# Optimization experiments

Hardware: AMD Instinct MI355X
Metric: run time of the kernel (lower is better)

## Reference

```python
import jax, jax.numpy as jnp
import numpy as np

N = 50000          # nodes in current snapshot
NUM = 20000        # nodes persisting from past snapshots (args.number[now-past])
PAST = 3           # history length
D = 128            # first_dim == hidden_dim == out_dim (forced by W_his usage)
K1, K2 = 25, 10    # sampled neighbor fan-outs
ALPHA = 0.2        # LeakyReLU slope
EPS = 1e-12        # torch F.normalize eps


def _l2norm(x):
    n = jnp.sqrt(jnp.sum(x * x, axis=1, keepdims=True))
    return x / jnp.maximum(n, EPS)


def _leaky(x):
    return jax.nn.leaky_relu(x, ALPHA)


def _sage(x, neigh_idx, W):
    # mean over sampled neighbors, concat with self, single linear
    neigh = jnp.mean(x[neigh_idx], axis=1)            # [N, d_in]
    return jnp.concatenate([x, neigh], axis=1) @ W    # [N, d_out]


def _temporal_mean(feat_head, hist, W_his, W_T):
    # hist: [PAST, NUM, D]; mean of per-snapshot linear maps
    tf = jnp.einsum('pnd,de->ne', hist, W_his) / PAST  # [NUM, D]
    return jnp.concatenate([feat_head, tf], axis=1) @ W_T


def setup_inputs() -> dict:
    key = jax.random.key(0)
    ks = jax.random.split(key, 9)
    return {
        'feats': jax.random.normal(ks[0], (N, D), dtype=jnp.float32),
        'agg_neigh_list1': jax.random.randint(ks[1], (N, K1), 0, N),
        'agg_neigh_list2': jax.random.randint(ks[2], (N, K2), 0, N),
        'hist_hidden1': jax.random.normal(ks[3], (PAST, NUM, D), dtype=jnp.float32),
        'hist_hidden2': jax.random.normal(ks[4], (PAST, NUM, D), dtype=jnp.float32),
        'W1': jax.random.normal(ks[5], (2 * D, D), dtype=jnp.float32) * 0.05,
        'W2': jax.random.normal(ks[6], (2 * D, D), dtype=jnp.float32) * 0.05,
        'W_his': jax.random.normal(ks[7], (D, D), dtype=jnp.float32) * 0.05,
        'W_T': jax.random.normal(ks[8], (2 * D, D), dtype=jnp.float32) * 0.05,
    }


def reference(feats, agg_neigh_list1, agg_neigh_list2, hist_hidden1,
              hist_hidden2, W1, W2, W_his, W_T):
    # ---- first-order SAGE (dropout identity in eval) ----
    h1 = _l2norm(_leaky(_sage(feats, agg_neigh_list1, W1)))        # [N, D]
    # ---- temporal fusion on hidden1 (now >= past, type='mean') ----
    f1 = _l2norm(_leaky(_temporal_mean(h1[:NUM], hist_hidden1, W_his, W_T)))
    h1_copy = jnp.concatenate([f1, h1[NUM:]], axis=0)              # [N, D]
    # ---- second-order SAGE ----
    h2 = _l2norm(_leaky(_sage(h1_copy, agg_neigh_list2, W2)))      # [N, D]
    # ---- temporal fusion on hidden2 ----
    f2 = _l2norm(_leaky(_temporal_mean(h2[:NUM], hist_hidden2, W_his, W_T)))
    feat = jnp.concatenate([f2, h2[NUM:]], axis=0)                 # [N, D]
    return (h1, h2, feat)
```

## Files before the change

kernel.cpp:

```cpp
#include <hip/hip_runtime.h>
#include <hip/hip_bf16.h>

#define N_NODES 50000
#define NUM_P   20000
#define D_DIM   128
#define ALPHA_  0.2f
#define EPS_    1e-12f
#define NT      16

typedef __attribute__((ext_vector_type(8))) short bf16x8;
typedef __attribute__((ext_vector_type(4))) float f32x4;
typedef __attribute__((ext_vector_type(2))) float f32x2;

#if defined(__has_builtin)
#if __has_builtin(__builtin_amdgcn_cvt_pk_f32_fp8) && __has_builtin(__builtin_amdgcn_cvt_pk_fp8_f32)
#define HAVE_HW_FP8 1
#endif
#endif

__device__ __forceinline__ float4 f4zero() { return make_float4(0.f, 0.f, 0.f, 0.f); }

__device__ __forceinline__ void scale4(float4& v, const float s) {
    v.x *= s; v.y *= s; v.z *= s; v.w *= s;
}

__device__ __forceinline__ short f2bf(float f) {
    __hip_bfloat16 h = __float2bfloat16(f);
    return *reinterpret_cast<short*>(&h);
}

__device__ __forceinline__ float bf2f(short u) {
    union { unsigned i; float f; } c;
    c.i = ((unsigned)(unsigned short)u) << 16;
    return c.f;
}

__device__ __forceinline__ short4 pack4(const float4 v) {
    short4 s;
    s.x = f2bf(v.x); s.y = f2bf(v.y); s.z = f2bf(v.z); s.w = f2bf(v.w);
    return s;
}

__device__ __forceinline__ float fp8_sw_dec(unsigned b) {
    unsigned e = (b >> 3) & 0xF, m = b & 7;
    float v = (e == 0) ? (float)m * 0.001953125f
                       : __uint_as_float(((e + 120u) << 23) | (m << 20));
    return (b & 0x80) ? -v : v;
}

__device__ __forceinline__ unsigned fp8_sw_enc(float f) {
    unsigned s = f < 0.f ? 0x80u : 0u;
    float af = fabsf(f);
    if (af >= 448.f) return s | 0x7E;
    if (af < 0.0009765625f) return s;
    int e; float m = frexpf(af, &e);
    int E = e - 1;
    if (E < -6) {
        int q = (int)rintf(af * 512.f);
        if (q >= 8) return s | 0x08;
        return s | (unsigned)q;
    }
    int q = (int)rintf(m * 16.f);
    if (q == 16) { q = 8; ++E; }
    if (E > 8) return s | 0x7E;
    return s | ((unsigned)(E + 7) << 3) | (unsigned)(q - 8);
}

template<bool HI>
__device__ __forceinline__ f32x2 fp8x2_dec(unsigned v) {
#ifdef HAVE_HW_FP8
    return __builtin_amdgcn_cvt_pk_f32_fp8((int)v, HI);
#else
    f32x2 r;
    unsigned b0 = HI ? ((v >> 16) & 0xFF) : (v & 0xFF);
    unsigned b1 = HI ? (v >> 24)          : ((v >> 8) & 0xFF);
    r[0] = fp8_sw_dec(b0); r[1] = fp8_sw_dec(b1);
    return r;
#endif
}

__device__ __forceinline__ unsigned char f2fp8(float v) {
#ifdef HAVE_HW_FP8
    return (unsigned char)(__builtin_amdgcn_cvt_pk_fp8_f32(v, v, 0, false) & 0xFF);
#else
    return (unsigned char)fp8_sw_enc(v);
#endif
}

__device__ __forceinline__ unsigned pack4_fp8(const float4 v) {
#ifdef HAVE_HW_FP8
    int lo = __builtin_amdgcn_cvt_pk_fp8_f32(v.x, v.y, 0, false);
    return (unsigned)__builtin_amdgcn_cvt_pk_fp8_f32(v.z, v.w, lo, true);
#else
    return fp8_sw_enc(v.x) | (fp8_sw_enc(v.y) << 8) |
           (fp8_sw_enc(v.z) << 16) | (fp8_sw_enc(v.w) << 24);
#endif
}

__global__ __launch_bounds__(256)
void cvt_all_kernel(const float* __restrict__ W1, const float* __restrict__ W2,
                    const float* __restrict__ Whis, const float* __restrict__ WTm,
                    short* __restrict__ ow,
                    const float* __restrict__ feats, short* __restrict__ ob,
                    unsigned* __restrict__ o8)
{
    if (blockIdx.x < 448) {
        const int i = blockIdx.x * 256 + threadIdx.x;
        float v;
        if (i < 65536) {
            const float* W = (i < 32768) ? W1 : W2;
            const int t = i & 32767;
            v = W[(size_t)(t & 255) * D_DIM + (t >> 8)];
        } else if (i < 81920) {
            const int t = i - 65536;
            v = Whis[(size_t)(t & 127) * D_DIM + (t >> 7)];
        } else {
            const int t = i - 81920;
            v = WTm[(size_t)(t & 255) * D_DIM + (t >> 8)];
        }
        ow[i] = f2bf(v);
    } else {
        const int i = (blockIdx.x - 448) * 256 + threadIdx.x;
        const float4 v = reinterpret_cast<const float4*>(feats)[i];
        reinterpret_cast<short4*>(ob)[i] = pack4(v);
        o8[i] = pack4_fp8(v);
    }
}

__global__ __launch_bounds__(256)
void fcvt_kernel(const float* __restrict__ in, short* __restrict__ ob)
{
    const int i = blockIdx.x * 256 + threadIdx.x;
    const float4 v = reinterpret_cast<const float4*>(in)[i];
    reinterpret_cast<short4*>(ob)[i] = pack4(v);
}

template<int K>
__global__ __launch_bounds__(256)
void sage_f8(const short*    __restrict__ srcB,
             const unsigned* __restrict__ src8,
             const int*      __restrict__ idx,
             const short*    __restrict__ WTg,
             float* __restrict__ out0,
             short* __restrict__ outb, int nb_limit,
             unsigned char* __restrict__ out8, int n8_limit,
             float* __restrict__ out1)
{
    __shared__ __align__(16) char uni[NT * 132 * 4];
    __shared__ float rnorm[NT];
    __shared__ int   sidx[NT * K];
    short* xs = reinterpret_cast<short*>(uni);
    float* ys = reinterpret_cast<float*>(uni);

    const int tid  = threadIdx.x;
    const int base = blockIdx.x * NT;

    for (int i = tid; i < NT * K; i += 256)
        sidx[i] = idx[(size_t)base * K + i];
    __syncthreads();

    {
        const int n = tid >> 4;
        const int l = tid & 15;
        const int node = base + n;
        const int swzn = (n & 7) << 3;

        const int4 s8 = reinterpret_cast<const int4*>(srcB + (size_t)node * D_DIM)[l];

        float a0 = 0.f, a1 = 0.f, a2 = 0.f, a3 = 0.f;
        float a4 = 0.f, a5 = 0.f, a6 = 0.f, a7 = 0.f;
        for (int k = 0; k < K; ++k) {
            const int r = sidx[n * K + k];
            const uint2 v = *reinterpret_cast<const uint2*>(src8 + (size_t)r * 32 + l * 2);
            const f32x2 p0 = fp8x2_dec<false>(v.x);
            const f32x2 p1 = fp8x2_dec<true>(v.x);
            const f32x2 p2 = fp8x2_dec<false>(v.y);
            const f32x2 p3 = fp8x2_dec<true>(v.y);
            a0 += p0[0]; a1 += p0[1]; a2 += p1[0]; a3 += p1[1];
            a4 += p2[0]; a5 += p2[1]; a6 += p3[0]; a7 += p3[1];
        }
        const float s = 1.0f / (float)K;
        short m8[8];
        m8[0] = f2bf(a0 * s); m8[1] = f2bf(a1 * s); m8[2] = f2bf(a2 * s); m8[3] = f2bf(a3 * s);
        m8[4] = f2bf(a4 * s); m8[5] = f2bf(a5 * s); m8[6] = f2bf(a6 * s); m8[7] = f2bf(a7 * s);

        *reinterpret_cast<int4*>(&xs[n * 256 + ((l * 8) ^ swzn)])         = s8;
        *reinterpret_cast<int4*>(&xs[n * 256 + ((D_DIM + l * 8) ^ swzn)]) = *reinterpret_cast<int4*>(m8);
    }
    __syncthreads();

    const int w    = tid >> 6;
    const int l    = tid & 63;
    const int arow = l & 15;
    const int kg   = l >> 4;
    const int swz  = (arow & 7) << 3;

    f32x4 acc0 = {0.f, 0.f, 0.f, 0.f};
    f32x4 acc1 = {0.f, 0.f, 0.f, 0.f};
    const int colbase = w * 32;
    const short* b0 = WTg + (size_t)(colbase + arow) * 256 + kg * 8;
    const short* b1 = b0 + 16 * 256;

    #pragma unroll
    for (int step = 0; step < 8; ++step) {
        const int aoff = arow * 256 + ((step * 32 + kg * 8) ^ swz);
        const bf16x8 av  = *reinterpret_cast<const bf16x8*>(&xs[aoff]);
        const bf16x8 bv0 = *reinterpret_cast<const bf16x8*>(b0 + step * 32);
        const bf16x8 bv1 = *reinterpret_cast<const bf16x8*>(b1 + step * 32);
        acc0 = __builtin_amdgcn_mfma_f32_16x16x32_bf16(av, bv0, acc0, 0, 0, 0);
        acc1 = __builtin_amdgcn_mfma_f32_16x16x32_bf16(av, bv1, acc1, 0, 0, 0);
    }
    __syncthreads();

    {
        const int r0 = kg * 4;
        #pragma unroll
        for (int r = 0; r < 4; ++r) {
            float v0 = acc0[r]; v0 = v0 > 0.f ? v0 : ALPHA_ * v0;
            float v1 = acc1[r]; v1 = v1 > 0.f ? v1 : ALPHA_ * v1;
            ys[(r0 + r) * 132 + colbase + arow]      = v0;
            ys[(r0 + r) * 132 + colbase + 16 + arow] = v1;
        }
    }
    __syncthreads();

    {
        const int n  = tid >> 4;
        const int ll = tid & 15;
        float s = 0.f;
        #pragma unroll
        for (int jj = 0; jj < D_DIM; jj += 16) { const float t = ys[n * 132 + ll + jj]; s += t * t; }
        #pragma unroll
        for (int o = 8; o > 0; o >>= 1) s += __shfl_xor(s, o);
        if (ll == 0) rnorm[n] = 1.0f / fmaxf(sqrtf(s), EPS_);
    }
    __syncthreads();

    {
        const int j = tid & 127;
        const int g = tid >> 7;
        #pragma unroll
        for (int r = 0; r < 8; ++r) {
            const int n    = g * 8 + r;
            const int node = base + n;
            const float v  = ys[n * 132 + j] * rnorm[n];
            out0[(size_t)node * D_DIM + j] = v;
            if (outb != nullptr && node < nb_limit) outb[(size_t)node * D_DIM + j] = f2bf(v);
            if (out8 != nullptr && node < n8_limit) out8[(size_t)node * D_DIM + j] = f2fp8(v);
            if (out1 != nullptr && node >= NUM_P)   out1[(size_t)node * D_DIM + j] = v;
        }
    }
}

template<int K>
__global__ __launch_bounds__(256)
void sage_mfma8(const short* __restrict__ src,
                const int*   __restrict__ idx,
                const short* __restrict__ WTg,
                float* __restrict__ out0,
                short* __restrict__ outb,
                int nb_limit,
                float* __restrict__ out1)
{
    __shared__ __align__(16) char uni[NT * 132 * 4];
    __shared__ float rnorm[NT];
    __shared__ int   sidx[NT * K];
    short* xs = reinterpret_cast<short*>(uni);
    float* ys = reinterpret_cast<float*>(uni);

    const int tid  = threadIdx.x;
    const int base = blockIdx.x * NT;

    for (int i = tid; i < NT * K; i += 256)
        sidx[i] = idx[(size_t)base * K + i];
    __syncthreads();

    {
        const int gp = tid >> 5;
        const int l  = tid & 31;
        for (int n = gp; n < NT; n += 8) {
            const int node = base + n;
            const short4 s4 = reinterpret_cast<const short4*>(src + (size_t)node * D_DIM)[l];
            float4 a4 = f4zero();
            for (int k = 0; k < K; ++k) {
                const int r = sidx[n * K + k];
                const short4 v4 = reinterpret_cast<const short4*>(src + (size_t)r * D_DIM)[l];
                a4.x += bf2f(v4.x); a4.y += bf2f(v4.y);
                a4.z += bf2f(v4.z); a4.w += bf2f(v4.w);
            }
            scale4(a4, 1.0f / (float)K);
            const int swzn = (n & 7) << 3;
            *reinterpret_cast<short4*>(&xs[n * 256 + ((l * 4) ^ swzn)])         = s4;
            *reinterpret_cast<short4*>(&xs[n * 256 + ((D_DIM + l * 4) ^ swzn)]) = pack4(a4);
        }
    }
    __syncthreads();

    const int w    = tid >> 6;
    const int l    = tid & 63;
    const int arow = l & 15;
    const int kg   = l >> 4;
    const int swz  = (arow & 7) << 3;

    f32x4 acc0 = {0.f, 0.f, 0.f, 0.f};
    f32x4 acc1 = {0.f, 0.f, 0.f, 0.f};
    const int colbase = w * 32;
    const short* b0 = WTg + (size_t)(colbase + arow) * 256 + kg * 8;
    const short* b1 = b0 + 16 * 256;

    #pragma unroll
    for (int step = 0; step < 8; ++step) {
        const int aoff = arow * 256 + ((step * 32 + kg * 8) ^ swz);
        const bf16x8 av  = *reinterpret_cast<const bf16x8*>(&xs[aoff]);
        const bf16x8 bv0 = *reinterpret_cast<const bf16x8*>(b0 + step * 32);
        const bf16x8 bv1 = *reinterpret_cast<const bf16x8*>(b1 + step * 32);
        acc0 = __builtin_amdgcn_mfma_f32_16x16x32_bf16(av, bv0, acc0, 0, 0, 0);
        acc1 = __builtin_amdgcn_mfma_f32_16x16x32_bf16(av, bv1, acc1, 0, 0, 0);
    }
    __syncthreads();

    {
        const int r0 = kg * 4;
        #pragma unroll
        for (int r = 0; r < 4; ++r) {
            float v0 = acc0[r]; v0 = v0 > 0.f ? v0 : ALPHA_ * v0;
            float v1 = acc1[r]; v1 = v1 > 0.f ? v1 : ALPHA_ * v1;
            ys[(r0 + r) * 132 + colbase + arow]      = v0;
            ys[(r0 + r) * 132 + colbase + 16 + arow] = v1;
        }
    }
    __syncthreads();

    {
        const int n  = tid >> 4;
        const int ll = tid & 15;
        float s = 0.f;
        #pragma unroll
        for (int jj = 0; jj < D_DIM; jj += 16) { const float t = ys[n * 132 + ll + jj]; s += t * t; }
        #pragma unroll
        for (int o = 8; o > 0; o >>= 1) s += __shfl_xor(s, o);
        if (ll == 0) rnorm[n] = 1.0f / fmaxf(sqrtf(s), EPS_);
    }
    __syncthreads();

    {
        const int j = tid & 127;
        const int g = tid >> 7;
        #pragma unroll
        for (int r = 0; r < 8; ++r) {
            const int n    = g * 8 + r;
            const int node = base + n;
            const float v  = ys[n * 132 + j] * rnorm[n];
            out0[(size_t)node * D_DIM + j] = v;
            if (outb != nullptr && node < nb_limit) outb[(size_t)node * D_DIM + j] = f2bf(v);
            if (out1 != nullptr && node >= NUM_P)   out1[(size_t)node * D_DIM + j] = v;
        }
    }
}

__global__ __launch_bounds__(256)
void temporal_mfma(const short* headb,
                   const float* __restrict__ hist,
                   const short* __restrict__ WhisTg,
                   const short* __restrict__ WTTg,
                   float* __restrict__ outp,
                   short* outb,
                   unsigned char* out8)
{
    __shared__ __align__(16) char uni[NT * 132 * 4];
    __shared__ float rnorm[NT];
    short* xs = reinterpret_cast<short*>(uni);
    float* ys = reinterpret_cast<float*>(uni);

    const int tid  = threadIdx.x;
    const int base = blockIdx.x * NT;
    const size_t HS = (size_t)NUM_P * D_DIM;

    {
        const int gp = tid >> 5;
        const int l  = tid & 31;
        for (int n = gp; n < NT; n += 8) {
            const size_t off = (size_t)(base + n) * D_DIM;
            const short4 h4 = reinterpret_cast<const short4*>(headb + off)[l];
            const float4 p0 = reinterpret_cast<const float4*>(hist + off)[l];
            const float4 p1 = reinterpret_cast<const float4*>(hist + off + HS)[l];
            const float4 p2 = reinterpret_cast<const float4*>(hist + off + 2 * HS)[l];
            float4 m4;
            m4.x = (p0.x + p1.x + p2.x) * (1.0f / 3.0f);
            m4.y = (p0.y + p1.y + p2.y) * (1.0f / 3.0f);
            m4.z = (p0.z + p1.z + p2.z) * (1.0f / 3.0f);
            m4.w = (p0.w + p1.w + p2.w) * (1.0f / 3.0f);
            const int swzn = (n & 7) << 3;
            *reinterpret_cast<short4*>(&xs[n * 256 + ((l * 4) ^ swzn)])         = h4;
            *reinterpret_cast<short4*>(&xs[n * 256 + ((D_DIM + l * 4) ^ swzn)]) = pack4(m4);
        }
    }
    __syncthreads();

    const int w    = tid >> 6;
    const int l    = tid & 63;
    const int arow = l & 15;
    const int kg   = l >> 4;
    const int swz  = (arow & 7) << 3;
    const int colbase = w * 32;

    {
        f32x4 t0 = {0.f, 0.f, 0.f, 0.f};
        f32x4 t1 = {0.f, 0.f, 0.f, 0.f};
        const short* b0 = WhisTg + (size_t)(colbase + arow) * 128 + kg * 8;
        const short* b1 = b0 + 16 * 128;
        #pragma unroll
        for (int step = 0; step < 4; ++step) {
            const int aoff = arow * 256 + ((D_DIM + step * 32 + kg * 8) ^ swz);
            const bf16x8 av  = *reinterpret_cast<const bf16x8*>(&xs[aoff]);
            const bf16x8 bv0 = *reinterpret_cast<const bf16x8*>(b0 + step * 32);
            const bf16x8 bv1 = *reinterpret_cast<const bf16x8*>(b1 + step * 32);
            t0 = __builtin_amdgcn_mfma_f32_16x16x32_bf16(av, bv0, t0, 0, 0, 0);
            t1 = __builtin_amdgcn_mfma_f32_16x16x32_bf16(av, bv1, t1, 0, 0, 0);
        }
        __syncthreads();

        #pragma unroll
        for (int r = 0; r < 4; ++r) {
            const int node = kg * 4 + r;
            const int swzn = (node & 7) << 3;
            xs[node * 256 + ((D_DIM + colbase + arow) ^ swzn)]      = f2bf(t0[r]);
            xs[node * 256 + ((D_DIM + colbase + 16 + arow) ^ swzn)] = f2bf(t1[r]);
        }
    }
    __syncthreads();

    f32x4 acc0 = {0.f, 0.f, 0.f, 0.f};
    f32x4 acc1 = {0.f, 0.f, 0.f, 0.f};
    {
        const short* b0 = WTTg + (size_t)(colbase + arow) * 256 + kg * 8;
        const short* b1 = b0 + 16 * 256;
        #pragma unroll
        for (int step = 0; step < 8; ++step) {
            const int aoff = arow * 256 + ((step * 32 + kg * 8) ^ swz);
            const bf16x8 av  = *reinterpret_cast<const bf16x8*>(&xs[aoff]);
            const bf16x8 bv0 = *reinterpret_cast<const bf16x8*>(b0 + step * 32);
            const bf16x8 bv1 = *reinterpret_cast<const bf16x8*>(b1 + step * 32);
            acc0 = __builtin_amdgcn_mfma_f32_16x16x32_bf16(av, bv0, acc0, 0, 0, 0);
            acc1 = __builtin_amdgcn_mfma_f32_16x16x32_bf16(av, bv1, acc1, 0, 0, 0);
        }
    }
    __syncthreads();

    {
        const int r0 = kg * 4;
        #pragma unroll
        for (int r = 0; r < 4; ++r) {
            float v0 = acc0[r]; v0 = v0 > 0.f ? v0 : ALPHA_ * v0;
            float v1 = acc1[r]; v1 = v1 > 0.f ? v1 : ALPHA_ * v1;
            ys[(r0 + r) * 132 + colbase + arow]      = v0;
            ys[(r0 + r) * 132 + colbase + 16 + arow] = v1;
        }
    }
    __syncthreads();

    {
        const int n  = tid >> 4;
        const int ll = tid & 15;
        float s = 0.f;
        #pragma unroll
        for (int jj = 0; jj < D_DIM; jj += 16) { const float t = ys[n * 132 + ll + jj]; s += t * t; }
        #pragma unroll
        for (int o = 8; o > 0; o >>= 1) s += __shfl_xor(s, o);
        if (ll == 0) rnorm[n] = 1.0f / fmaxf(sqrtf(s), EPS_);
    }
    __syncthreads();

    {
        const int j = tid & 127;
        const int g = tid >> 7;
        #pragma unroll
        for (int r = 0; r < 8; ++r) {
            const int n = g * 8 + r;
            const float v = ys[n * 132 + j] * rnorm[n];
            const size_t o = (size_t)(base + n) * D_DIM + j;
            if (outp != nullptr) outp[o] = v;
            if (outb != nullptr) outb[o] = f2bf(v);
            if (out8 != nullptr) out8[o] = f2fp8(v);
        }
    }
}

__global__ __launch_bounds__(256)
void temporal_v8(const float* __restrict__ head,
                 const float* __restrict__ hist,
                 const float* __restrict__ Whis,
                 const float* __restrict__ WTm,
                 float* __restrict__ outp,
                 short* __restrict__ outb)
{
    __shared__ float xs[NT][2 * D_DIM];
    __shared__ float hm[NT][D_DIM];
    __shared__ float rnorm[NT];

    const int tid  = threadIdx.x;
    const int base = blockIdx.x * NT;
    const size_t HS = (size_t)NUM_P * D_DIM;

    {
        const int gp = tid >> 5;
        const int l  = tid & 31;
        for (int n = gp; n < NT; n += 8) {
            const size_t off = (size_t)(base + n) * D_DIM;
            const float4 h4 = reinterpret_cast<const float4*>(head + off)[l];
            const float4 p0 = reinterpret_cast<const float4*>(hist + off)[l];
            const float4 p1 = reinterpret_cast<const float4*>(hist + off + HS)[l];
            const float4 p2 = reinterpret_cast<const float4*>(hist + off + 2 * HS)[l];
            float4 m4;
            m4.x = (p0.x + p1.x + p2.x) * (1.0f / 3.0f);
            m4.y = (p0.y + p1.y + p2.y) * (1.0f / 3.0f);
            m4.z = (p0.z + p1.z + p2.z) * (1.0f / 3.0f);
            m4.w = (p0.w + p1.w + p2.w) * (1.0f / 3.0f);
            reinterpret_cast<float4*>(&xs[n][0])[l] = h4;
            reinterpret_cast<float4*>(&hm[n][0])[l] = m4;
        }
    }
    __syncthreads();

    const int j  = tid & 127;
    const int g  = tid >> 7;
    const int nb = g * 8;

    {
        float a2[8];
        #pragma unroll
        for (int r = 0; r < 8; ++r) a2[r] = 0.f;
        for (int c4 = 0; c4 < D_DIM / 4; ++c4) {
            const int c = c4 * 4;
            const float w0 = Whis[(size_t)(c + 0) * D_DIM + j];
            const float w1 = Whis[(size_t)(c + 1) * D_DIM + j];
            const float w2 = Whis[(size_t)(c + 2) * D_DIM + j];
            const float w3 = Whis[(size_t)(c + 3) * D_DIM + j];
            #pragma unroll
            for (int r = 0; r < 8; ++r) {
                const float4 xv = *reinterpret_cast<const float4*>(&hm[nb + r][c]);
                a2[r] = fmaf(xv.w, w3, fmaf(xv.z, w2, fmaf(xv.y, w1, fmaf(xv.x, w0, a2[r]))));
            }
        }
        __syncthreads();
        #pragma unroll
        for (int r = 0; r < 8; ++r) xs[nb + r][D_DIM + j] = a2[r];
    }
    __syncthreads();

    float acc[8];
    #pragma unroll
    for (int r = 0; r < 8; ++r) acc[r] = 0.f;
    for (int c4 = 0; c4 < (2 * D_DIM) / 4; ++c4) {
        const int c = c4 * 4;
        const float w0 = WTm[(size_t)(c + 0) * D_DIM + j];
        const float w1 = WTm[(size_t)(c + 1) * D_DIM + j];
        const float w2 = WTm[(size_t)(c + 2) * D_DIM + j];
        const float w3 = WTm[(size_t)(c + 3) * D_DIM + j];
        #pragma unroll
        for (int r = 0; r < 8; ++r) {
            const float4 xv = *reinterpret_cast<const float4*>(&xs[nb + r][c]);
            acc[r] = fmaf(xv.w, w3, fmaf(xv.z, w2, fmaf(xv.y, w1, fmaf(xv.x, w0, acc[r]))));
        }
    }
    __syncthreads();

    #pragma unroll
    for (int r = 0; r < 8; ++r) {
        float v = acc[r];
        v = v > 0.f ? v : ALPHA_ * v;
        xs[nb + r][j] = v;
    }
    __syncthreads();

    {
        const int n  = tid >> 4;
        const int ll = tid & 15;
        float s = 0.f;
        #pragma unroll
        for (int jj = ll; jj < D_DIM; jj += 16) { const float t = xs[n][jj]; s += t * t; }
        #pragma unroll
        for (int o = 8; o > 0; o >>= 1) s += __shfl_xor(s, o);
        if (ll == 0) rnorm[n] = 1.0f / fmaxf(sqrtf(s), EPS_);
    }
    __syncthreads();

    #pragma unroll
    for (int r = 0; r < 8; ++r) {
        const int n = nb + r;
        const float v = xs[n][j] * rnorm[n];
        const size_t o = (size_t)(base + n) * D_DIM + j;
        if (outp != nullptr) outp[o] = v;
        if (outb != nullptr) outb[o] = f2bf(v);
    }
}

template<int K, bool SPLIT>
__global__ __launch_bounds__(256)
void sage_v5(const float* __restrict__ srcLow,
             const float* __restrict__ srcHigh,
             const int*   __restrict__ idx,
             const float* __restrict__ W,
             float* __restrict__ out0,
             float* __restrict__ out1)
{
    __shared__ float xs[NT][2 * D_DIM];
    __shared__ int   sidx[NT * K];
    __shared__ float rnorm[NT];

    const int tid  = threadIdx.x;
    const int base = blockIdx.x * NT;

    for (int i = tid; i < NT * K; i += 256)
        sidx[i] = idx[(size_t)base * K + i];
    __syncthreads();

    {
        const int gp = tid >> 5;
        const int l  = tid & 31;
        for (int n = gp; n < NT; n += 8) {
            const int node = base + n;
            const float* sp = (!SPLIT || node < NUM_P) ? srcLow : srcHigh;
            const float4 s4 = reinterpret_cast<const float4*>(sp + (size_t)node * D_DIM)[l];
            float4 a4 = f4zero();
            for (int k = 0; k < K; ++k) {
                const int r = sidx[n * K + k];
                const float* rp = (!SPLIT || r < NUM_P) ? srcLow : srcHigh;
                const float4 v4 = reinterpret_cast<const float4*>(rp + (size_t)r * D_DIM)[l];
                a4.x += v4.x; a4.y += v4.y; a4.z += v4.z; a4.w += v4.w;
            }
            scale4(a4, 1.0f / (float)K);
            reinterpret_cast<float4*>(&xs[n][0])[l]     = s4;
            reinterpret_cast<float4*>(&xs[n][D_DIM])[l] = a4;
        }
    }
    __syncthreads();

    const int j  = tid & 127;
    const int g  = tid >> 7;
    const int nb = g * 8;

    float acc[8];
    #pragma unroll
    for (int r = 0; r < 8; ++r) acc[r] = 0.f;
    for (int c4 = 0; c4 < (2 * D_DIM) / 4; ++c4) {
        const int c = c4 * 4;
        const float w0 = W[(size_t)(c + 0) * D_DIM + j];
        const float w1 = W[(size_t)(c + 1) * D_DIM + j];
        const float w2 = W[(size_t)(c + 2) * D_DIM + j];
        const float w3 = W[(size_t)(c + 3) * D_DIM + j];
        #pragma unroll
        for (int r = 0; r < 8; ++r) {
            const float4 xv = *reinterpret_cast<const float4*>(&xs[nb + r][c]);
            acc[r] = fmaf(xv.w, w3, fmaf(xv.z, w2, fmaf(xv.y, w1, fmaf(xv.x, w0, acc[r]))));
        }
    }
    __syncthreads();

    #pragma unroll
    for (int r = 0; r < 8; ++r) {
        float v = acc[r];
        v = v > 0.f ? v : ALPHA_ * v;
        xs[nb + r][j] = v;
    }
    __syncthreads();

    {
        const int n  = tid >> 4;
        const int ll = tid & 15;
        float s = 0.f;
        #pragma unroll
        for (int jj = ll; jj < D_DIM; jj += 16) { const float t = xs[n][jj]; s += t * t; }
        #pragma unroll
        for (int o = 8; o > 0; o >>= 1) s += __shfl_xor(s, o);
        if (ll == 0) rnorm[n] = 1.0f / fmaxf(sqrtf(s), EPS_);
    }
    __syncthreads();

    #pragma unroll
    for (int r = 0; r < 8; ++r) {
        const int n    = nb + r;
        const int node = base + n;
        const float v  = xs[n][j] * rnorm[n];
        out0[(size_t)node * D_DIM + j] = v;
        if (out1 != nullptr && node >= NUM_P) out1[(size_t)node * D_DIM + j] = v;
    }
}

extern "C" void kernel_launch(void* const* d_in, const int* in_sizes, int n_in,
                              void* d_out, int out_size, void* d_ws, size_t ws_size,
                              hipStream_t stream)
{
    (void)in_sizes; (void)n_in; (void)out_size;

    const float* feats = (const float*)d_in[0];
    const int*   idx1  = (const int*)  d_in[1];
    const int*   idx2  = (const int*)  d_in[2];
    const float* hist1 = (const float*)d_in[3];
    const float* hist2 = (const float*)d_in[4];
    const float* W1    = (const float*)d_in[5];
    const float* W2    = (const float*)d_in[6];
    const float* Whis  = (const float*)d_in[7];
    const float* WTm   = (const float*)d_in[8];

    float* out = (float*)d_out;
    float* h1o = out;
    float* h2o = out + (size_t)N_NODES * D_DIM;
    float* fo  = out + 2 * (size_t)N_NODES * D_DIM;

    const int sage_blocks = N_NODES / NT;
    const int temp_blocks = NUM_P   / NT;

    const size_t SZ_N  = (size_t)N_NODES * D_DIM;
    const size_t SZ_P  = (size_t)NUM_P  * D_DIM;
    const size_t WOFF  = 114688;
    const size_t needF8 = (WOFF + 2 * SZ_N + SZ_P) * 2 + 2 * SZ_N;
    const size_t needA  = (WOFF + 2 * SZ_N + SZ_P) * 2;

    short* wsp  = (short*)d_ws;
    short* W1T  = wsp;
    short* W2T  = wsp + 32768;
    short* WhT  = wsp + 65536;
    short* WTT  = wsp + 81920;
    short* fb   = wsp + WOFF;
    short* hb   = fb + SZ_N;
    short* h2b  = hb + SZ_N;
    unsigned* f8 = (unsigned*)(h2b + SZ_P);
    unsigned* h8 = f8 + SZ_N / 4;

    if (ws_size >= needF8) {
        cvt_all_kernel<<<448 + (int)(SZ_N / 1024), 256, 0, stream>>>(
            W1, W2, Whis, WTm, wsp, feats, fb, f8);

        sage_f8<25><<<sage_blocks, 256, 0, stream>>>(
            fb, f8, idx1, W1T, h1o, hb, N_NODES, (unsigned char*)h8, N_NODES, nullptr);
        temporal_mfma<<<temp_blocks, 256, 0, stream>>>(
            hb, hist1, WhT, WTT, nullptr, hb, (unsigned char*)h8);
        sage_f8<10><<<sage_blocks, 256, 0, stream>>>(
            hb, h8, idx2, W2T, h2o, h2b, NUM_P, nullptr, 0, fo);
        temporal_mfma<<<temp_blocks, 256, 0, stream>>>(
            h2b, hist2, WhT, WTT, fo, nullptr, nullptr);
    } else if (ws_size >= needA) {
        cvt_all_kernel<<<448, 256, 0, stream>>>(W1, W2, Whis, WTm, wsp, feats, fb, f8);
        fcvt_kernel<<<(int)(SZ_N / 1024), 256, 0, stream>>>(feats, fb);

        sage_mfma8<25><<<sage_blocks, 256, 0, stream>>>(fb, idx1, W1T, h1o, hb, N_NODES, nullptr);
        temporal_mfma<<<temp_blocks, 256, 0, stream>>>(hb, hist1, WhT, WTT, nullptr, hb, nullptr);
        sage_mfma8<10><<<sage_blocks, 256, 0, stream>>>(hb, idx2, W2T, h2o, h2b, NUM_P, fo);
        temporal_mfma<<<temp_blocks, 256, 0, stream>>>(h2b, hist2, WhT, WTT, fo, nullptr, nullptr);
    } else {
        sage_v5<25, false><<<sage_blocks, 256, 0, stream>>>(feats, feats, idx1, W1, h1o, nullptr);
        temporal_v8<<<temp_blocks, 256, 0, stream>>>(h1o, hist1, Whis, WTm, fo, nullptr);
        sage_v5<10, true><<<sage_blocks, 256, 0, stream>>>(fo, h1o, idx2, W2, h2o, fo);
        temporal_v8<<<temp_blocks, 256, 0, stream>>>(h2o, hist2, Whis, WTm, fo, nullptr);
    }
}
```

Baseline: 132.7 us.

## Fuse temporal fusion into SAGE kernels for persistent-node blocks

Folds the temporal-mean stage into the SAGE kernel. Blocks covering the first NUM_P nodes now go straight on to the history mean, the W_his and W_T MFMA GEMMs and the normalization while the fresh SAGE output is still in shared memory. This drops two kernel launches and the bf16 round-trip of the head rows through global memory. In exchange, the blocks holding persistent nodes do more work than the others, which may cause load imbalance. The extra code may also raise register pressure in the fused kernel.

```diff
diff --git a/kernel.cpp b/kernel.cpp
--- a/kernel.cpp
+++ b/kernel.cpp
@@ -137,14 +137,18 @@
 
 template<int K>
 __global__ __launch_bounds__(256)
-void sage_f8(const short*    __restrict__ srcB,
-             const unsigned* __restrict__ src8,
-             const int*      __restrict__ idx,
-             const short*    __restrict__ WTg,
-             float* __restrict__ out0,
-             short* __restrict__ outb, int nb_limit,
-             unsigned char* __restrict__ out8, int n8_limit,
-             float* __restrict__ out1)
+void sage_fused(const short*    __restrict__ srcB,
+                const unsigned* __restrict__ src8,
+                const int*      __restrict__ idx,
+                const short*    __restrict__ WTg,
+                const float*    __restrict__ hist,
+                const short*    __restrict__ WhisTg,
+                const short*    __restrict__ WTTg,
+                float* __restrict__ out0,
+                float* __restrict__ tail1,
+                short* __restrict__ tb,
+                unsigned char* __restrict__ t8,
+                float* __restrict__ tout)
 {
     __shared__ __align__(16) char uni[NT * 132 * 4];
     __shared__ float rnorm[NT];
@@ -194,25 +198,23 @@
     const int arow = l & 15;
     const int kg   = l >> 4;
     const int swz  = (arow & 7) << 3;
-
-    f32x4 acc0 = {0.f, 0.f, 0.f, 0.f};
-    f32x4 acc1 = {0.f, 0.f, 0.f, 0.f};
     const int colbase = w * 32;
-    const short* b0 = WTg + (size_t)(colbase + arow) * 256 + kg * 8;
-    const short* b1 = b0 + 16 * 256;
-
-    #pragma unroll
-    for (int step = 0; step < 8; ++step) {
-        const int aoff = arow * 256 + ((step * 32 + kg * 8) ^ swz);
-        const bf16x8 av  = *reinterpret_cast<const bf16x8*>(&xs[aoff]);
-        const bf16x8 bv0 = *reinterpret_cast<const bf16x8*>(b0 + step * 32);
-        const bf16x8 bv1 = *reinterpret_cast<const bf16x8*>(b1 + step * 32);
-        acc0 = __builtin_amdgcn_mfma_f32_16x16x32_bf16(av, bv0, acc0, 0, 0, 0);
-        acc1 = __builtin_amdgcn_mfma_f32_16x16x32_bf16(av, bv1, acc1, 0, 0, 0);
-    }
-    __syncthreads();
-
-    {
+
+    {
+        f32x4 acc0 = {0.f, 0.f, 0.f, 0.f};
+        f32x4 acc1 = {0.f, 0.f, 0.f, 0.f};
+        const short* b0 = WTg + (size_t)(colbase + arow) * 256 + kg * 8;
+        const short* b1 = b0 + 16 * 256;
+        #pragma unroll
+        for (int step = 0; step < 8; ++step) {
+            const int aoff = arow * 256 + ((step * 32 + kg * 8) ^ swz);
+            const bf16x8 av  = *reinterpret_cast<const bf16x8*>(&xs[aoff]);
+            const bf16x8 bv0 = *reinterpret_cast<const bf16x8*>(b0 + step * 32);
+            const bf16x8 bv1 = *reinterpret_cast<const bf16x8*>(b1 + step * 32);
+            acc0 = __builtin_amdgcn_mfma_f32_16x16x32_bf16(av, bv0, acc0, 0, 0, 0);
+            acc1 = __builtin_amdgcn_mfma_f32_16x16x32_bf16(av, bv1, acc1, 0, 0, 0);
+        }
+        __syncthreads();
         const int r0 = kg * 4;
         #pragma unroll
         for (int r = 0; r < 4; ++r) {
@@ -236,18 +238,260 @@
     }
     __syncthreads();
 
+    const int j = tid & 127;
+    const int g = tid >> 7;
+    float vout[8];
+    #pragma unroll
+    for (int r = 0; r < 8; ++r) {
+        const int n = g * 8 + r;
+        vout[r] = ys[n * 132 + j] * rnorm[n];
+    }
+    #pragma unroll
+    for (int r = 0; r < 8; ++r)
+        out0[(size_t)(base + g * 8 + r) * D_DIM + j] = vout[r];
+
+    const bool temp = (hist != nullptr) && (base < NUM_P);
+
+    if (!temp) {
+        #pragma unroll
+        for (int r = 0; r < 8; ++r) {
+            const int node = base + g * 8 + r;
+            const size_t o = (size_t)node * D_DIM + j;
+            if (node >= NUM_P) {
+                if (tail1 != nullptr) tail1[o] = vout[r];
+                if (tb != nullptr) tb[o] = f2bf(vout[r]);
+                if (t8 != nullptr) t8[o] = f2fp8(vout[r]);
+            } else {
+                if (tb != nullptr) tb[o] = f2bf(vout[r]);
+                if (t8 != nullptr) t8[o] = f2fp8(vout[r]);
+            }
+        }
+        return;
+    }
+
+    __syncthreads();
+
+    #pragma unroll
+    for (int r = 0; r < 8; ++r) {
+        const int n = g * 8 + r;
+        const int swzn = (n & 7) << 3;
+        xs[n * 256 + (j ^ swzn)] = f2bf(vout[r]);
+    }
+    {
+        const int gp = tid >> 5;
+        const int ll = tid & 31;
+        const size_t HS = (size_t)NUM_P * D_DIM;
+        for (int n = gp; n < NT; n += 8) {
+            const size_t off = (size_t)(base + n) * D_DIM;
+            const float4 p0 = reinterpret_cast<const float4*>(hist + off)[ll];
+            const float4 p1 = reinterpret_cast<const float4*>(hist + off + HS)[ll];
+            const float4 p2 = reinterpret_cast<const float4*>(hist + off + 2 * HS)[ll];
+            float4 m4;
+            m4.x = (p0.x + p1.x + p2.x) * (1.0f / 3.0f);
+            m4.y = (p0.y + p1.y + p2.y) * (1.0f / 3.0f);
+            m4.z = (p0.z + p1.z + p2.z) * (1.0f / 3.0f);
+            m4.w = (p0.w + p1.w + p2.w) * (1.0f / 3.0f);
+            const int swzn = (n & 7) << 3;
+            *reinterpret_cast<short4*>(&xs[n * 256 + ((D_DIM + ll * 4) ^ swzn)]) = pack4(m4);
+        }
+    }
+    __syncthreads();
+
+    {
+        f32x4 t0 = {0.f, 0.f, 0.f, 0.f};
+        f32x4 t1 = {0.f, 0.f, 0.f, 0.f};
+        const short* b0 = WhisTg + (size_t)(colbase + arow) * 128 + kg * 8;
+        const short* b1 = b0 + 16 * 128;
+        #pragma unroll
+        for (int step = 0; step < 4; ++step) {
+            const int aoff = arow * 256 + ((D_DIM + step * 32 + kg * 8) ^ swz);
+            const bf16x8 av  = *reinterpret_cast<const bf16x8*>(&xs[aoff]);
+            const bf16x8 bv0 = *reinterpret_cast<const bf16x8*>(b0 + step * 32);
+            const bf16x8 bv1 = *reinterpret_cast<const bf16x8*>(b1 + step * 32);
+            t0 = __builtin_amdgcn_mfma_f32_16x16x32_bf16(av, bv0, t0, 0, 0, 0);
+            t1 = __builtin_amdgcn_mfma_f32_16x16x32_bf16(av, bv1, t1, 0, 0, 0);
+        }
+        __syncthreads();
+        #pragma unroll
+        for (int r = 0; r < 4; ++r) {
+            const int node = kg * 4 + r;
+            const int swzn = (node & 7) << 3;
+            xs[node * 256 + ((D_DIM + colbase + arow) ^ swzn)]      = f2bf(t0[r]);
+            xs[node * 256 + ((D_DIM + colbase + 16 + arow) ^ swzn)] = f2bf(t1[r]);
+        }
+    }
+    __syncthreads();
+
+    {
+        f32x4 acc0 = {0.f, 0.f, 0.f, 0.f};
+        f32x4 acc1 = {0.f, 0.f, 0.f, 0.f};
+        const short* b0 = WTTg + (size_t)(colbase + arow) * 256 + kg * 8;
+        const short* b1 = b0 + 16 * 256;
+        #pragma unroll
+        for (int step = 0; step < 8; ++step) {
+            const int aoff = arow * 256 + ((step * 32 + kg * 8) ^ swz);
+            const bf16x8 av  = *reinterpret_cast<const bf16x8*>(&xs[aoff]);
+            const bf16x8 bv0 = *reinterpret_cast<const bf16x8*>(b0 + step * 32);
+            const bf16x8 bv1 = *reinterpret_cast<const bf16x8*>(b1 + step * 32);
+            acc0 = __builtin_amdgcn_mfma_f32_16x16x32_bf16(av, bv0, acc0, 0, 0, 0);
+            acc1 = __builtin_amdgcn_mfma_f32_16x16x32_bf16(av, bv1, acc1, 0, 0, 0);
+        }
+        __syncthreads();
+        const int r0 = kg * 4;
+        #pragma unroll
+        for (int r = 0; r < 4; ++r) {
+            float v0 = acc0[r]; v0 = v0 > 0.f ? v0 : ALPHA_ * v0;
+            float v1 = acc1[r]; v1 = v1 > 0.f ? v1 : ALPHA_ * v1;
+            ys[(r0 + r) * 132 + colbase + arow]      = v0;
+            ys[(r0 + r) * 132 + colbase + 16 + arow] = v1;
+        }
+    }
+    __syncthreads();
+
+    {
+        const int n  = tid >> 4;
+        const int ll = tid & 15;
+        float s = 0.f;
+        #pragma unroll
+        for (int jj = 0; jj < D_DIM; jj += 16) { const float t = ys[n * 132 + ll + jj]; s += t * t; }
+        #pragma unroll
+        for (int o = 8; o > 0; o >>= 1) s += __shfl_xor(s, o);
+        if (ll == 0) rnorm[n] = 1.0f / fmaxf(sqrtf(s), EPS_);
+    }
+    __syncthreads();
+
+    #pragma unroll
+    for (int r = 0; r < 8; ++r) {
+        const int n = g * 8 + r;
+        const float v = ys[n * 132 + j] * rnorm[n];
+        const size_t o = (size_t)(base + n) * D_DIM + j;
+        if (tout != nullptr) tout[o] = v;
+        if (tb != nullptr) tb[o] = f2bf(v);
+        if (t8 != nullptr) t8[o] = f2fp8(v);
+    }
+}
+
+__global__ __launch_bounds__(256)
+void temporal_mfma(const short* headb,
+                   const float* __restrict__ hist,
+                   const short* __restrict__ WhisTg,
+                   const short* __restrict__ WTTg,
+                   float* __restrict__ outp,
+                   short* outb)
+{
+    __shared__ __align__(16) char uni[NT * 132 * 4];
+    __shared__ float rnorm[NT];
+    short* xs = reinterpret_cast<short*>(uni);
+    float* ys = reinterpret_cast<float*>(uni);
+
+    const int tid  = threadIdx.x;
+    const int base = blockIdx.x * NT;
+    const size_t HS = (size_t)NUM_P * D_DIM;
+
+    {
+        const int gp = tid >> 5;
+        const int l  = tid & 31;
+        for (int n = gp; n < NT; n += 8) {
+            const size_t off = (size_t)(base + n) * D_DIM;
+            const short4 h4 = reinterpret_cast<const short4*>(headb + off)[l];
+            const float4 p0 = reinterpret_cast<const float4*>(hist + off)[l];
+            const float4 p1 = reinterpret_cast<const float4*>(hist + off + HS)[l];
+            const float4 p2 = reinterpret_cast<const float4*>(hist + off + 2 * HS)[l];
+            float4 m4;
+            m4.x = (p0.x + p1.x + p2.x) * (1.0f / 3.0f);
+            m4.y = (p0.y + p1.y + p2.y) * (1.0f / 3.0f);
+            m4.z = (p0.z + p1.z + p2.z) * (1.0f / 3.0f);
+            m4.w = (p0.w + p1.w + p2.w) * (1.0f / 3.0f);
+            const int swzn = (n & 7) << 3;
+            *reinterpret_cast<short4*>(&xs[n * 256 + ((l * 4) ^ swzn)])         = h4;
+            *reinterpret_cast<short4*>(&xs[n * 256 + ((D_DIM + l * 4) ^ swzn)]) = pack4(m4);
+        }
+    }
+    __syncthreads();
+
+    const int w    = tid >> 6;
+    const int l    = tid & 63;
+    const int arow = l & 15;
+    const int kg   = l >> 4;
+    const int swz  = (arow & 7) << 3;
+    const int colbase = w * 32;
+
+    {
+        f32x4 t0 = {0.f, 0.f, 0.f, 0.f};
+        f32x4 t1 = {0.f, 0.f, 0.f, 0.f};
+        const short* b0 = WhisTg + (size_t)(colbase + arow) * 128 + kg * 8;
+        const short* b1 = b0 + 16 * 128;
+        #pragma unroll
+        for (int step = 0; step < 4; ++step) {
+            const int aoff = arow * 256 + ((D_DIM + step * 32 + kg * 8) ^ swz);
+            const bf16x8 av  = *reinterpret_cast<const bf16x8*>(&xs[aoff]);
+            const bf16x8 bv0 = *reinterpret_cast<const bf16x8*>(b0 + step * 32);
+            const bf16x8 bv1 = *reinterpret_cast<const bf16x8*>(b1 + step * 32);
+            t0 = __builtin_amdgcn_mfma_f32_16x16x32_bf16(av, bv0, t0, 0, 0, 0);
+            t1 = __builtin_amdgcn_mfma_f32_16x16x32_bf16(av, bv1, t1, 0, 0, 0);
+        }
+        __syncthreads();
+        #pragma unroll
+        for (int r = 0; r < 4; ++r) {
+            const int node = kg * 4 + r;
+            const int swzn = (node & 7) << 3;
+            xs[node * 256 + ((D_DIM + colbase + arow) ^ swzn)]      = f2bf(t0[r]);
+            xs[node * 256 + ((D_DIM + colbase + 16 + arow) ^ swzn)] = f2bf(t1[r]);
+        }
+    }
+    __syncthreads();
+
+    f32x4 acc0 = {0.f, 0.f, 0.f, 0.f};
+    f32x4 acc1 = {0.f, 0.f, 0.f, 0.f};
+    {
+        const short* b0 = WTTg + (size_t)(colbase + arow) * 256 + kg * 8;
+        const short* b1 = b0 + 16 * 256;
+        #pragma unroll
+        for (int step = 0; step < 8; ++step) {
+            const int aoff = arow * 256 + ((step * 32 + kg * 8) ^ swz);
+            const bf16x8 av  = *reinterpret_cast<const bf16x8*>(&xs[aoff]);
+            const bf16x8 bv0 = *reinterpret_cast<const bf16x8*>(b0 + step * 32);
+            const bf16x8 bv1 = *reinterpret_cast<const bf16x8*>(b1 + step * 32);
+            acc0 = __builtin_amdgcn_mfma_f32_16x16x32_bf16(av, bv0, acc0, 0, 0, 0);
+            acc1 = __builtin_amdgcn_mfma_f32_16x16x32_bf16(av, bv1, acc1, 0, 0, 0);
+        }
+    }
+    __syncthreads();
+
+    {
+        const int r0 = kg * 4;
+        #pragma unroll
+        for (int r = 0; r < 4; ++r) {
+            float v0 = acc0[r]; v0 = v0 > 0.f ? v0 : ALPHA_ * v0;
+            float v1 = acc1[r]; v1 = v1 > 0.f ? v1 : ALPHA_ * v1;
+            ys[(r0 + r) * 132 + colbase + arow]      = v0;
+            ys[(r0 + r) * 132 + colbase + 16 + arow] = v1;
+        }
+    }
+    __syncthreads();
+
+    {
+        const int n  = tid >> 4;
+        const int ll = tid & 15;
+        float s = 0.f;
+        #pragma unroll
+        for (int jj = 0; jj < D_DIM; jj += 16) { const float t = ys[n * 132 + ll + jj]; s += t * t; }
+        #pragma unroll
+        for (int o = 8; o > 0; o >>= 1) s += __shfl_xor(s, o);
+        if (ll == 0) rnorm[n] = 1.0f / fmaxf(sqrtf(s), EPS_);
+    }
+    __syncthreads();
+
     {
         const int j = tid & 127;
         const int g = tid >> 7;
         #pragma unroll
         for (int r = 0; r < 8; ++r) {
-            const int n    = g * 8 + r;
-            const int node = base + n;
-            const float v  = ys[n * 132 + j] * rnorm[n];
-            out0[(size_t)node * D_DIM + j] = v;
-            if (outb != nullptr && node < nb_limit) outb[(size_t)node * D_DIM + j] = f2bf(v);
-            if (out8 != nullptr && node < n8_limit) out8[(size_t)node * D_DIM + j] = f2fp8(v);
-            if (out1 != nullptr && node >= NUM_P)   out1[(size_t)node * D_DIM + j] = v;
+            const int n = g * 8 + r;
+            const float v = ys[n * 132 + j] * rnorm[n];
+            const size_t o = (size_t)(base + n) * D_DIM + j;
+            if (outp != nullptr) outp[o] = v;
+            if (outb != nullptr) outb[o] = f2bf(v);
         }
     }
 }
@@ -359,134 +603,6 @@
 }
 
 __global__ __launch_bounds__(256)
-void temporal_mfma(const short* headb,
-                   const float* __restrict__ hist,
-                   const short* __restrict__ WhisTg,
-                   const short* __restrict__ WTTg,
-                   float* __restrict__ outp,
-                   short* outb,
-                   unsigned char* out8)
-{
-    __shared__ __align__(16) char uni[NT * 132 * 4];
-    __shared__ float rnorm[NT];
-    short* xs = reinterpret_cast<short*>(uni);
-    float* ys = reinterpret_cast<float*>(uni);
-
-    const int tid  = threadIdx.x;
-    const int base = blockIdx.x * NT;
-    const size_t HS = (size_t)NUM_P * D_DIM;
-
-    {
-        const int gp = tid >> 5;
-        const int l  = tid & 31;
-        for (int n = gp; n < NT; n += 8) {
-            const size_t off = (size_t)(base + n) * D_DIM;
-            const short4 h4 = reinterpret_cast<const short4*>(headb + off)[l];
-            const float4 p0 = reinterpret_cast<const float4*>(hist + off)[l];
-            const float4 p1 = reinterpret_cast<const float4*>(hist + off + HS)[l];
-            const float4 p2 = reinterpret_cast<const float4*>(hist + off + 2 * HS)[l];
-            float4 m4;
-            m4.x = (p0.x + p1.x + p2.x) * (1.0f / 3.0f);
-            m4.y = (p0.y + p1.y + p2.y) * (1.0f / 3.0f);
-            m4.z = (p0.z + p1.z + p2.z) * (1.0f / 3.0f);
-            m4.w = (p0.w + p1.w + p2.w) * (1.0f / 3.0f);
-            const int swzn = (n & 7) << 3;
-            *reinterpret_cast<short4*>(&xs[n * 256 + ((l * 4) ^ swzn)])         = h4;
-            *reinterpret_cast<short4*>(&xs[n * 256 + ((D_DIM + l * 4) ^ swzn)]) = pack4(m4);
-        }
-    }
-    __syncthreads();
-
-    const int w    = tid >> 6;
-    const int l    = tid & 63;
-    const int arow = l & 15;
-    const int kg   = l >> 4;
-    const int swz  = (arow & 7) << 3;
-    const int colbase = w * 32;
-
-    {
-        f32x4 t0 = {0.f, 0.f, 0.f, 0.f};
-        f32x4 t1 = {0.f, 0.f, 0.f, 0.f};
-        const short* b0 = WhisTg + (size_t)(colbase + arow) * 128 + kg * 8;
-        const short* b1 = b0 + 16 * 128;
-        #pragma unroll
-        for (int step = 0; step < 4; ++step) {
-            const int aoff = arow * 256 + ((D_DIM + step * 32 + kg * 8) ^ swz);
-            const bf16x8 av  = *reinterpret_cast<const bf16x8*>(&xs[aoff]);
-            const bf16x8 bv0 = *reinterpret_cast<const bf16x8*>(b0 + step * 32);
-            const bf16x8 bv1 = *reinterpret_cast<const bf16x8*>(b1 + step * 32);
-            t0 = __builtin_amdgcn_mfma_f32_16x16x32_bf16(av, bv0, t0, 0, 0, 0);
-            t1 = __builtin_amdgcn_mfma_f32_16x16x32_bf16(av, bv1, t1, 0, 0, 0);
-        }
-        __syncthreads();
-
-        #pragma unroll
-        for (int r = 0; r < 4; ++r) {
-            const int node = kg * 4 + r;
-            const int swzn = (node & 7) << 3;
-            xs[node * 256 + ((D_DIM + colbase + arow) ^ swzn)]      = f2bf(t0[r]);
-            xs[node * 256 + ((D_DIM + colbase + 16 + arow) ^ swzn)] = f2bf(t1[r]);
-        }
-    }
-    __syncthreads();
-
-    f32x4 acc0 = {0.f, 0.f, 0.f, 0.f};
-    f32x4 acc1 = {0.f, 0.f, 0.f, 0.f};
-    {
-        const short* b0 = WTTg + (size_t)(colbase + arow) * 256 + kg * 8;
-        const short* b1 = b0 + 16 * 256;
-        #pragma unroll
-        for (int step = 0; step < 8; ++step) {
-            const int aoff = arow * 256 + ((step * 32 + kg * 8) ^ swz);
-            const bf16x8 av  = *reinterpret_cast<const bf16x8*>(&xs[aoff]);
-            const bf16x8 bv0 = *reinterpret_cast<const bf16x8*>(b0 + step * 32);
-            const bf16x8 bv1 = *reinterpret_cast<const bf16x8*>(b1 + step * 32);
-            acc0 = __builtin_amdgcn_mfma_f32_16x16x32_bf16(av, bv0, acc0, 0, 0, 0);
-            acc1 = __builtin_amdgcn_mfma_f32_16x16x32_bf16(av, bv1, acc1, 0, 0, 0);
-        }
-    }
-    __syncthreads();
-
-    {
-        const int r0 = kg * 4;
-        #pragma unroll
-        for (int r = 0; r < 4; ++r) {
-            float v0 = acc0[r]; v0 = v0 > 0.f ? v0 : ALPHA_ * v0;
-            float v1 = acc1[r]; v1 = v1 > 0.f ? v1 : ALPHA_ * v1;
-            ys[(r0 + r) * 132 + colbase + arow]      = v0;
-            ys[(r0 + r) * 132 + colbase + 16 + arow] = v1;
-        }
-    }
-    __syncthreads();
-
-    {
-        const int n  = tid >> 4;
-        const int ll = tid & 15;
-        float s = 0.f;
-        #pragma unroll
-        for (int jj = 0; jj < D_DIM; jj += 16) { const float t = ys[n * 132 + ll + jj]; s += t * t; }
-        #pragma unroll
-        for (int o = 8; o > 0; o >>= 1) s += __shfl_xor(s, o);
-        if (ll == 0) rnorm[n] = 1.0f / fmaxf(sqrtf(s), EPS_);
-    }
-    __syncthreads();
-
-    {
-        const int j = tid & 127;
-        const int g = tid >> 7;
-        #pragma unroll
-        for (int r = 0; r < 8; ++r) {
-            const int n = g * 8 + r;
-            const float v = ys[n * 132 + j] * rnorm[n];
-            const size_t o = (size_t)(base + n) * D_DIM + j;
-            if (outp != nullptr) outp[o] = v;
-            if (outb != nullptr) outb[o] = f2bf(v);
-            if (out8 != nullptr) out8[o] = f2fp8(v);
-        }
-    }
-}
-
-__global__ __launch_bounds__(256)
 void temporal_v8(const float* __restrict__ head,
                  const float* __restrict__ hist,
                  const float* __restrict__ Whis,
@@ -732,22 +848,21 @@
         cvt_all_kernel<<<448 + (int)(SZ_N / 1024), 256, 0, stream>>>(
             W1, W2, Whis, WTm, wsp, feats, fb, f8);
 
-        sage_f8<25><<<sage_blocks, 256, 0, stream>>>(
-            fb, f8, idx1, W1T, h1o, hb, N_NODES, (unsigned char*)h8, N_NODES, nullptr);
-        temporal_mfma<<<temp_blocks, 256, 0, stream>>>(
-            hb, hist1, WhT, WTT, nullptr, hb, (unsigned char*)h8);
-        sage_f8<10><<<sage_blocks, 256, 0, stream>>>(
-            hb, h8, idx2, W2T, h2o, h2b, NUM_P, nullptr, 0, fo);
-        temporal_mfma<<<temp_blocks, 256, 0, stream>>>(
-            h2b, hist2, WhT, WTT, fo, nullptr, nullptr);
+        sage_fused<25><<<sage_blocks, 256, 0, stream>>>(
+            fb, f8, idx1, W1T, hist1, WhT, WTT,
+            h1o, nullptr, hb, (unsigned char*)h8, nullptr);
+
+        sage_fused<10><<<sage_blocks, 256, 0, stream>>>(
+            hb, h8, idx2, W2T, hist2, WhT, WTT,
+            h2o, fo, nullptr, nullptr, fo);
     } else if (ws_size >= needA) {
         cvt_all_kernel<<<448, 256, 0, stream>>>(W1, W2, Whis, WTm, wsp, feats, fb, f8);
         fcvt_kernel<<<(int)(SZ_N / 1024), 256, 0, stream>>>(feats, fb);
 
         sage_mfma8<25><<<sage_blocks, 256, 0, stream>>>(fb, idx1, W1T, h1o, hb, N_NODES, nullptr);
-        temporal_mfma<<<temp_blocks, 256, 0, stream>>>(hb, hist1, WhT, WTT, nullptr, hb, nullptr);
+        temporal_mfma<<<temp_blocks, 256, 0, stream>>>(hb, hist1, WhT, WTT, nullptr, hb);
         sage_mfma8<10><<<sage_blocks, 256, 0, stream>>>(hb, idx2, W2T, h2o, h2b, NUM_P, fo);
-        temporal_mfma<<<temp_blocks, 256, 0, stream>>>(h2b, hist2, WhT, WTT, fo, nullptr, nullptr);
+        temporal_mfma<<<temp_blocks, 256, 0, stream>>>(h2b, hist2, WhT, WTT, fo, nullptr);
     } else {
         sage_v5<25, false><<<sage_blocks, 256, 0, stream>>>(feats, feats, idx1, W1, h1o, nullptr);
         temporal_v8<<<temp_blocks, 256, 0, stream>>>(h1o, hist1, Whis, WTm, fo, nullptr);
```

New measurement: 117.1 us. 11.8% less time.
